# Performance work log

Measured on AMD Instinct MI355X. Metric: run time of the kernel, lower is better.

## Reference

```python
import jax, jax.numpy as jnp
import numpy as np

# SamplesLoss(loss='sinkhorn', p=1, blur=0.05): entropic regularization eps = blur**p = 0.05,
# debiased Sinkhorn divergence S(a,b) = OT(a,b) - 0.5*OT(a,a) - 0.5*OT(b,b).
EPS = 0.05
N_ITER = 50
N_POINTS = 32


def _cost(X, Y):
    # p=1 cost: Euclidean distance. X:[B,N,D] Y:[B,M,D] -> [B,N,M]
    d2 = jnp.sum((X[:, :, None, :] - Y[:, None, :, :]) ** 2, axis=-1)
    return jnp.sqrt(d2 + 1e-12)


def _ot(X, Y):
    # log-domain Sinkhorn with uniform weights; returns dual cost <mu,f>+<nu,g> per batch.
    B, N, _ = X.shape
    M = Y.shape[1]
    C = _cost(X, Y)  # [B,N,M]
    log_mu = jnp.full((B, N), -np.log(N), C.dtype)
    log_nu = jnp.full((B, M), -np.log(M), C.dtype)

    def body(carry, _):
        f, g = carry
        f = -EPS * jax.nn.logsumexp((g[:, None, :] - C) / EPS + log_nu[:, None, :], axis=2)
        g = -EPS * jax.nn.logsumexp((f[:, :, None] - C) / EPS + log_mu[:, :, None], axis=1)
        return (f, g), None

    init = (jnp.zeros((B, N), C.dtype), jnp.zeros((B, M), C.dtype))
    (f, g), _ = jax.lax.scan(body, init, None, length=N_ITER)
    return jnp.mean(f, axis=-1) + jnp.mean(g, axis=-1)  # uniform weights => mean


def _sinkhorn_div(X, Y):
    return _ot(X, Y) - 0.5 * _ot(X, X) - 0.5 * _ot(Y, Y)


def _encode(x, W, edge_index):
    # simple 1-layer GCN-style encoder: linear + mean neighbor aggregation + self, ReLU
    h = x @ W  # [n_nodes, emb_dim]
    src, dst = edge_index[0], edge_index[1]
    n = x.shape[0]
    agg = jax.ops.segment_sum(h[src], dst, num_segments=n)
    deg = jax.ops.segment_sum(jnp.ones(src.shape, h.dtype), dst, num_segments=n)
    return jax.nn.relu(h + agg / jnp.maximum(deg, 1.0)[:, None])


def setup_inputs() -> dict:
    key = jax.random.key(0)
    k1, k2, k3, k4, k5 = jax.random.split(key, 5)
    n_nodes, d_feat, emb_dim = 50000, 128, 256
    n_edges, n_pairs = 800000, 8192
    x = jax.random.normal(k1, (n_nodes, d_feat), jnp.float32)
    W = jax.random.normal(k2, (d_feat, emb_dim), jnp.float32) / np.sqrt(d_feat)
    edge_index = jax.random.randint(k3, (2, n_edges), 0, n_nodes, jnp.int64)
    pairs = jax.random.randint(k4, (2, n_pairs), 0, n_nodes, jnp.int64)
    graph_dist = jax.random.uniform(k5, (n_pairs,), jnp.float32, 1.0, 5.0)
    return {"x": x, "W": W, "edge_index": edge_index, "pairs": pairs,
            "graph_dist": graph_dist}


def reference(x, W, edge_index, pairs, graph_dist):
    z = _encode(x, W, edge_index)                       # [n_nodes, emb_dim]
    B = pairs.shape[1]
    Xa = z[pairs[0]].reshape(B, N_POINTS, -1)           # [B, n_points, space_dim]
    Xb = z[pairs[1]].reshape(B, N_POINTS, -1)
    distance = _sinkhorn_div(Xa, Xb)                    # = -score_pairs
    distortion = jnp.abs(distance - graph_dist) / graph_dist
    return jnp.mean(distortion)
```

## Files before the change

### kernel.cpp

```cpp
#include <hip/hip_runtime.h>

#define N_NODES 50000
#define N_EDGES 800000
#define N_PAIRS 8192
#define N_SLOTS (2 * N_PAIRS)
#define CAP     64

#define INV_EPS   20.0f
#define LOG2E_F   1.4426950408889634f
#define LN2_F     0.6931471805599453f
#define LN32_F    3.4657359027997265f
#define EPS_F     0.05f

typedef float f2 __attribute__((ext_vector_type(2)));

__global__ void k_mark(const int* __restrict__ pairs, int* __restrict__ flags) {
    int t = blockIdx.x * 256 + threadIdx.x;
    if (t < N_SLOTS) flags[pairs[t]] = 1;
}

__global__ __launch_bounds__(256) void k_scatter(
        const int* __restrict__ eidx, const int* __restrict__ flags,
        int* __restrict__ cnt, int* __restrict__ bucket) {
    int t = blockIdx.x * 256 + threadIdx.x;
    int dst = eidx[N_EDGES + t];
    if (!flags[dst]) return;
    int pos = atomicAdd(&cnt[dst], 1);
    if (pos < CAP) bucket[dst * CAP + pos] = eidx[t];
}

__global__ __launch_bounds__(256) void k_gemm(
        const int* __restrict__ pairs, const float* __restrict__ x,
        const int* __restrict__ cnt, const int* __restrict__ bucket,
        const float* __restrict__ W, float* __restrict__ Z) {
    __shared__ __align__(16) float Us[16 * 128];
    int sbase = blockIdx.x * 16;
    int t = threadIdx.x;
    int wave = t >> 6, lane = t & 63;

    #pragma unroll
    for (int rr = 0; rr < 4; ++rr) {
        int r = wave * 4 + rr;
        int node = pairs[sbase + r];
        int n = cnt[node];
        int m = (n < CAP) ? n : CAP;
        const int* bk = bucket + node * CAP;
        float ax = 0.0f, ay = 0.0f;
        int k = 0;
        for (; k + 4 <= m; k += 4) {
            int s0 = bk[k], s1 = bk[k + 1], s2 = bk[k + 2], s3 = bk[k + 3];
            float2 v0 = *(const float2*)(x + (size_t)s0 * 128 + lane * 2);
            float2 v1 = *(const float2*)(x + (size_t)s1 * 128 + lane * 2);
            float2 v2 = *(const float2*)(x + (size_t)s2 * 128 + lane * 2);
            float2 v3 = *(const float2*)(x + (size_t)s3 * 128 + lane * 2);
            ax += (v0.x + v1.x) + (v2.x + v3.x);
            ay += (v0.y + v1.y) + (v2.y + v3.y);
        }
        for (; k < m; ++k) {
            int s0 = bk[k];
            float2 v0 = *(const float2*)(x + (size_t)s0 * 128 + lane * 2);
            ax += v0.x;
            ay += v0.y;
        }
        float rdeg = 1.0f / fmaxf((float)n, 1.0f);
        float2 xv = *(const float2*)(x + (size_t)node * 128 + lane * 2);
        float2 o;
        o.x = fmaf(ax, rdeg, xv.x);
        o.y = fmaf(ay, rdeg, xv.y);
        *(float2*)(Us + r * 128 + lane * 2) = o;
    }
    __syncthreads();

    int jq = t & 63;
    int rq = t >> 6;
    float acc[4][4] = {};
    const float4* Wv = (const float4*)W;

    for (int k4 = 0; k4 < 32; ++k4) {
        float4 wv[4];
        #pragma unroll
        for (int i = 0; i < 4; ++i) wv[i] = Wv[(size_t)(k4 * 4 + i) * 64 + jq];
        #pragma unroll
        for (int r = 0; r < 4; ++r) {
            float4 uv = *(const float4*)(Us + (rq * 4 + r) * 128 + k4 * 4);
            float uk0 = uv.x, uk1 = uv.y, uk2 = uv.z, uk3 = uv.w;
            acc[r][0] = fmaf(uk0, wv[0].x, acc[r][0]);
            acc[r][1] = fmaf(uk0, wv[0].y, acc[r][1]);
            acc[r][2] = fmaf(uk0, wv[0].z, acc[r][2]);
            acc[r][3] = fmaf(uk0, wv[0].w, acc[r][3]);
            acc[r][0] = fmaf(uk1, wv[1].x, acc[r][0]);
            acc[r][1] = fmaf(uk1, wv[1].y, acc[r][1]);
            acc[r][2] = fmaf(uk1, wv[1].z, acc[r][2]);
            acc[r][3] = fmaf(uk1, wv[1].w, acc[r][3]);
            acc[r][0] = fmaf(uk2, wv[2].x, acc[r][0]);
            acc[r][1] = fmaf(uk2, wv[2].y, acc[r][1]);
            acc[r][2] = fmaf(uk2, wv[2].z, acc[r][2]);
            acc[r][3] = fmaf(uk2, wv[2].w, acc[r][3]);
            acc[r][0] = fmaf(uk3, wv[3].x, acc[r][0]);
            acc[r][1] = fmaf(uk3, wv[3].y, acc[r][1]);
            acc[r][2] = fmaf(uk3, wv[3].z, acc[r][2]);
            acc[r][3] = fmaf(uk3, wv[3].w, acc[r][3]);
        }
    }

    #pragma unroll
    for (int r = 0; r < 4; ++r) {
        float4 o;
        o.x = fmaxf(acc[r][0], 0.0f);
        o.y = fmaxf(acc[r][1], 0.0f);
        o.z = fmaxf(acc[r][2], 0.0f);
        o.w = fmaxf(acc[r][3], 0.0f);
        *(float4*)(Z + (size_t)(sbase + rq * 4 + r) * 256 + jq * 4) = o;
    }
}

__global__ __launch_bounds__(256) void k_sinkhorn(
        const float* __restrict__ Z, float* __restrict__ dist) {
    __shared__ __align__(16) float smem[4][640];

    int w = threadIdx.x >> 6;
    int lane = threadIdx.x & 63;
    const float CSCALE = -INV_EPS * LOG2E_F;
    const float CBIAS  = -LN32_F * LOG2E_F;

    if (blockIdx.x < 2048) {
        float* sX = &smem[w][0];
        float* sY = &smem[w][256];
        float* sf = &smem[w][512];
        float* sg = &smem[w][544];
        float* su = &smem[w][576];
        float* sv = &smem[w][608];

        int b = blockIdx.x * 4 + w;
        int sx = b, sy = N_PAIRS + b;

        *(float4*)(&sX[lane * 4]) = ((const float4*)(Z + (size_t)sx * 256))[lane];
        *(float4*)(&sY[lane * 4]) = ((const float4*)(Z + (size_t)sy * 256))[lane];
        sg[lane & 31] = 0.0f;

        int i_r = lane & 31, jh = lane >> 5;
        int j_c = lane & 31, ih = lane >> 5;

        f2 CrowV[8], CcolV[8];
        {
            const f2* xp = (const f2*)(&sX[i_r * 8]);
            f2 x0 = xp[0], x1 = xp[1], x2 = xp[2], x3 = xp[3];
            #pragma unroll
            for (int t = 0; t < 16; ++t) {
                int j = jh * 16 + t;
                const f2* yp = (const f2*)(&sY[j * 8]);
                f2 d, s2;
                d = x0 - yp[0]; s2 = d * d;
                d = x1 - yp[1]; s2 = __builtin_elementwise_fma(d, d, s2);
                d = x2 - yp[2]; s2 = __builtin_elementwise_fma(d, d, s2);
                d = x3 - yp[3]; s2 = __builtin_elementwise_fma(d, d, s2);
                float d2 = s2.x + s2.y + 1e-12f;
                CrowV[t >> 1][t & 1] = fmaf(__builtin_amdgcn_sqrtf(d2), CSCALE, CBIAS);
            }
            const f2* yp = (const f2*)(&sY[j_c * 8]);
            f2 y0 = yp[0], y1 = yp[1], y2 = yp[2], y3 = yp[3];
            #pragma unroll
            for (int t = 0; t < 16; ++t) {
                int i = ih * 16 + t;
                const f2* qp = (const f2*)(&sX[i * 8]);
                f2 d, s2;
                d = qp[0] - y0; s2 = d * d;
                d = qp[1] - y1; s2 = __builtin_elementwise_fma(d, d, s2);
                d = qp[2] - y2; s2 = __builtin_elementwise_fma(d, d, s2);
                d = qp[3] - y3; s2 = __builtin_elementwise_fma(d, d, s2);
                float d2 = s2.x + s2.y + 1e-12f;
                CcolV[t >> 1][t & 1] = fmaf(__builtin_amdgcn_sqrtf(d2), CSCALE, CBIAS);
            }
        }

        float ft = 0.0f, gt = 0.0f;

        #pragma unroll 1
        for (int it = 0; it < 2; ++it) {
            {
                const float4* gp = (const float4*)(&sg[jh * 16]);
                float4 G0 = gp[0], G1 = gp[1], G2 = gp[2], G3 = gp[3];
                f2 gv[8] = {f2{G0.x, G0.y}, f2{G0.z, G0.w}, f2{G1.x, G1.y}, f2{G1.z, G1.w},
                            f2{G2.x, G2.y}, f2{G2.z, G2.w}, f2{G3.x, G3.y}, f2{G3.z, G3.w}};
                f2 val[8], m2 = f2{-1e30f, -1e30f};
                #pragma unroll
                for (int t2 = 0; t2 < 8; ++t2) {
                    val[t2] = gv[t2] + CrowV[t2];
                    m2 = __builtin_elementwise_max(m2, val[t2]);
                }
                float m = fmaxf(m2.x, m2.y);
                m = fmaxf(m, __shfl_xor(m, 32));
                f2 mm = f2{m, m};
                float s0 = 0.0f, s1 = 0.0f;
                #pragma unroll
                for (int t2 = 0; t2 < 8; ++t2) {
                    f2 e = val[t2] - mm;
                    s0 += __builtin_amdgcn_exp2f(e.x);
                    s1 += __builtin_amdgcn_exp2f(e.y);
                }
                float s = s0 + s1;
                s += __shfl_xor(s, 32);
                ft = -(m + __builtin_amdgcn_logf(s));
            }
            sf[lane & 31] = ft;
            {
                const float4* fp = (const float4*)(&sf[ih * 16]);
                float4 F0 = fp[0], F1 = fp[1], F2 = fp[2], F3 = fp[3];
                f2 fv[8] = {f2{F0.x, F0.y}, f2{F0.z, F0.w}, f2{F1.x, F1.y}, f2{F1.z, F1.w},
                            f2{F2.x, F2.y}, f2{F2.z, F2.w}, f2{F3.x, F3.y}, f2{F3.z, F3.w}};
                f2 val[8], m2 = f2{-1e30f, -1e30f};
                #pragma unroll
                for (int t2 = 0; t2 < 8; ++t2) {
                    val[t2] = fv[t2] + CcolV[t2];
                    m2 = __builtin_elementwise_max(m2, val[t2]);
                }
                float m = fmaxf(m2.x, m2.y);
                m = fmaxf(m, __shfl_xor(m, 32));
                f2 mm = f2{m, m};
                float s0 = 0.0f, s1 = 0.0f;
                #pragma unroll
                for (int t2 = 0; t2 < 8; ++t2) {
                    f2 e = val[t2] - mm;
                    s0 += __builtin_amdgcn_exp2f(e.x);
                    s1 += __builtin_amdgcn_exp2f(e.y);
                }
                float s = s0 + s1;
                s += __shfl_xor(s, 32);
                gt = -(m + __builtin_amdgcn_logf(s));
            }
            sg[lane & 31] = gt;
        }

        f2 KR2[8], KC2[8];
        float ureg = 1.0f, vreg = 1.0f;

        auto absorb = [&]() {
            const float4* gp = (const float4*)(&sg[jh * 16]);
            float4 G0 = gp[0], G1 = gp[1], G2 = gp[2], G3 = gp[3];
            f2 gv[8] = {f2{G0.x, G0.y}, f2{G0.z, G0.w}, f2{G1.x, G1.y}, f2{G1.z, G1.w},
                        f2{G2.x, G2.y}, f2{G2.z, G2.w}, f2{G3.x, G3.y}, f2{G3.z, G3.w}};
            f2 ftv = f2{ft, ft};
            #pragma unroll
            for (int t2 = 0; t2 < 8; ++t2) {
                f2 a = (gv[t2] + CrowV[t2]) + ftv;
                KR2[t2].x = __builtin_amdgcn_exp2f(a.x);
                KR2[t2].y = __builtin_amdgcn_exp2f(a.y);
            }
            const float4* fp = (const float4*)(&sf[ih * 16]);
            float4 F0 = fp[0], F1 = fp[1], F2 = fp[2], F3 = fp[3];
            f2 fv[8] = {f2{F0.x, F0.y}, f2{F0.z, F0.w}, f2{F1.x, F1.y}, f2{F1.z, F1.w},
                        f2{F2.x, F2.y}, f2{F2.z, F2.w}, f2{F3.x, F3.y}, f2{F3.z, F3.w}};
            f2 gtv = f2{gt, gt};
            #pragma unroll
            for (int t2 = 0; t2 < 8; ++t2) {
                f2 a = (fv[t2] + CcolV[t2]) + gtv;
                KC2[t2].x = __builtin_amdgcn_exp2f(a.x);
                KC2[t2].y = __builtin_amdgcn_exp2f(a.y);
            }
            sv[lane & 31] = 1.0f;
            ureg = 1.0f;
            vreg = 1.0f;
        };

        const int blens[5] = {6, 6, 12, 12, 12};
        absorb();
        #pragma unroll 1
        for (int blk = 0; blk < 5; ++blk) {
            int L = blens[blk];
            #pragma unroll 2
            for (int s6 = 0; s6 < L; ++s6) {
                {
                    const float4* vp = (const float4*)(&sv[jh * 16]);
                    float4 A0 = vp[0], A1 = vp[1], A2 = vp[2], A3 = vp[3];
                    f2 acc0 = KR2[0] * f2{A0.x, A0.y};
                    f2 acc1 = KR2[1] * f2{A0.z, A0.w};
                    acc0 = __builtin_elementwise_fma(KR2[2], f2{A1.x, A1.y}, acc0);
                    acc1 = __builtin_elementwise_fma(KR2[3], f2{A1.z, A1.w}, acc1);
                    acc0 = __builtin_elementwise_fma(KR2[4], f2{A2.x, A2.y}, acc0);
                    acc1 = __builtin_elementwise_fma(KR2[5], f2{A2.z, A2.w}, acc1);
                    acc0 = __builtin_elementwise_fma(KR2[6], f2{A3.x, A3.y}, acc0);
                    acc1 = __builtin_elementwise_fma(KR2[7], f2{A3.z, A3.w}, acc1);
                    f2 a = acc0 + acc1;
                    float S = a.x + a.y;
                    S += __shfl_xor(S, 32);
                    ureg = __builtin_amdgcn_rcpf(S);
                }
                su[lane & 31] = ureg;
                {
                    const float4* up = (const float4*)(&su[ih * 16]);
                    float4 A0 = up[0], A1 = up[1], A2 = up[2], A3 = up[3];
                    f2 acc0 = KC2[0] * f2{A0.x, A0.y};
                    f2 acc1 = KC2[1] * f2{A0.z, A0.w};
                    acc0 = __builtin_elementwise_fma(KC2[2], f2{A1.x, A1.y}, acc0);
                    acc1 = __builtin_elementwise_fma(KC2[3], f2{A1.z, A1.w}, acc1);
                    acc0 = __builtin_elementwise_fma(KC2[4], f2{A2.x, A2.y}, acc0);
                    acc1 = __builtin_elementwise_fma(KC2[5], f2{A2.z, A2.w}, acc1);
                    acc0 = __builtin_elementwise_fma(KC2[6], f2{A3.x, A3.y}, acc0);
                    acc1 = __builtin_elementwise_fma(KC2[7], f2{A3.z, A3.w}, acc1);
                    f2 a = acc0 + acc1;
                    float T = a.x + a.y;
                    T += __shfl_xor(T, 32);
                    vreg = __builtin_amdgcn_rcpf(T);
                }
                sv[lane & 31] = vreg;
            }
            if (blk < 4) {
                ft += __builtin_amdgcn_logf(ureg);
                gt += __builtin_amdgcn_logf(vreg);
                sf[lane & 31] = ft;
                sg[lane & 31] = gt;
                absorb();
            }
        }
        ft += __builtin_amdgcn_logf(ureg);
        gt += __builtin_amdgcn_logf(vreg);

        float v = ft + gt;
        #pragma unroll
        for (int off = 32; off > 0; off >>= 1) v += __shfl_xor(v, off);
        if (lane == 0) {
            float cost = v * (EPS_F * LN2_F / 64.0f);
            unsafeAtomicAdd(&dist[b], cost);
        }
    } else {
        int h = lane >> 5, i = lane & 31;
        int P = (blockIdx.x - 2048) * 4 + w;
        int src = h ? (N_PAIRS + P) : P;

        float* sP  = &smem[w][h * 256];
        float* swv = &smem[w][512];
        float* spv = &smem[w][576];

        {
            const float4* zp = (const float4*)(Z + (size_t)src * 256);
            *(float4*)(&sP[i * 8])     = zp[i * 2];
            *(float4*)(&sP[i * 8 + 4]) = zp[i * 2 + 1];
        }

        f2 CV[16];
        {
            const f2* xp = (const f2*)(&sP[i * 8]);
            f2 x0 = xp[0], x1 = xp[1], x2 = xp[2], x3 = xp[3];
            #pragma unroll
            for (int j = 0; j < 32; ++j) {
                const f2* yp = (const f2*)(&sP[j * 8]);
                f2 d, s2;
                d = x0 - yp[0]; s2 = d * d;
                d = x1 - yp[1]; s2 = __builtin_elementwise_fma(d, d, s2);
                d = x2 - yp[2]; s2 = __builtin_elementwise_fma(d, d, s2);
                d = x3 - yp[3]; s2 = __builtin_elementwise_fma(d, d, s2);
                float d2 = s2.x + s2.y + 1e-12f;
                CV[j >> 1][j & 1] = fmaf(__builtin_amdgcn_sqrtf(d2), CSCALE, CBIAS);
            }
        }

        float pp = 0.0f, E = 1.0f, wcur = 1.0f, wprev = 1.0f;
        f2 KV[16];
        #pragma unroll
        for (int t = 0; t < 16; ++t) {
            KV[t].x = __builtin_amdgcn_exp2f(CV[t].x);
            KV[t].y = __builtin_amdgcn_exp2f(CV[t].y);
        }
        swv[lane] = 1.0f;

        const int blens[9] = {4, 12, 12, 12, 12, 12, 12, 12, 12};
        #pragma unroll 1
        for (int blk = 0; blk < 9; ++blk) {
            int L = blens[blk];
            #pragma unroll 2
            for (int s = 0; s < L; ++s) {
                const float4* wp = (const float4*)(&swv[h * 32]);
                float4 A0 = wp[0], A1 = wp[1], A2 = wp[2], A3 = wp[3];
                float4 A4 = wp[4], A5 = wp[5], A6 = wp[6], A7 = wp[7];
                f2 acc0 = KV[0] * f2{A0.x, A0.y};
                f2 acc1 = KV[1] * f2{A0.z, A0.w};
                acc0 = __builtin_elementwise_fma(KV[2],  f2{A1.x, A1.y}, acc0);
                acc1 = __builtin_elementwise_fma(KV[3],  f2{A1.z, A1.w}, acc1);
                acc0 = __builtin_elementwise_fma(KV[4],  f2{A2.x, A2.y}, acc0);
                acc1 = __builtin_elementwise_fma(KV[5],  f2{A2.z, A2.w}, acc1);
                acc0 = __builtin_elementwise_fma(KV[6],  f2{A3.x, A3.y}, acc0);
                acc1 = __builtin_elementwise_fma(KV[7],  f2{A3.z, A3.w}, acc1);
                acc0 = __builtin_elementwise_fma(KV[8],  f2{A4.x, A4.y}, acc0);
                acc1 = __builtin_elementwise_fma(KV[9],  f2{A4.z, A4.w}, acc1);
                acc0 = __builtin_elementwise_fma(KV[10], f2{A5.x, A5.y}, acc0);
                acc1 = __builtin_elementwise_fma(KV[11], f2{A5.z, A5.w}, acc1);
                acc0 = __builtin_elementwise_fma(KV[12], f2{A6.x, A6.y}, acc0);
                acc1 = __builtin_elementwise_fma(KV[13], f2{A6.z, A6.w}, acc1);
                acc0 = __builtin_elementwise_fma(KV[14], f2{A7.x, A7.y}, acc0);
                acc1 = __builtin_elementwise_fma(KV[15], f2{A7.z, A7.w}, acc1);
                f2 a = acc0 + acc1;
                float S = a.x + a.y;
                wprev = wcur;
                wcur = __builtin_amdgcn_rcpf(S) * E;
                swv[h * 32 + i] = wcur;
            }
            if (blk < 8) {
                pp += __builtin_amdgcn_logf(wcur);
                spv[lane] = pp;
                const float4* pv = (const float4*)(&spv[h * 32]);
                float4 P0 = pv[0], P1 = pv[1], P2 = pv[2], P3 = pv[3];
                float4 P4 = pv[4], P5 = pv[5], P6 = pv[6], P7 = pv[7];
                f2 pj[16] = {f2{P0.x,P0.y}, f2{P0.z,P0.w}, f2{P1.x,P1.y}, f2{P1.z,P1.w},
                             f2{P2.x,P2.y}, f2{P2.z,P2.w}, f2{P3.x,P3.y}, f2{P3.z,P3.w},
                             f2{P4.x,P4.y}, f2{P4.z,P4.w}, f2{P5.x,P5.y}, f2{P5.z,P5.w},
                             f2{P6.x,P6.y}, f2{P6.z,P6.w}, f2{P7.x,P7.y}, f2{P7.z,P7.w}};
                #pragma unroll
                for (int t = 0; t < 16; ++t) {
                    f2 a = pj[t] + CV[t];
                    KV[t].x = __builtin_amdgcn_exp2f(a.x);
                    KV[t].y = __builtin_amdgcn_exp2f(a.y);
                }
                E = __builtin_amdgcn_exp2f(-pp);
                wcur = 1.0f;
                swv[lane] = 1.0f;
            }
        }

        float zsum = 2.0f * pp + __builtin_amdgcn_logf(wprev)
                   + __builtin_amdgcn_logf(wcur);
        #pragma unroll
        for (int off = 16; off > 0; off >>= 1) zsum += __shfl_xor(zsum, off);
        if (i == 0) {
            float cost = zsum * (EPS_F * LN2_F / 32.0f);
            unsafeAtomicAdd(&dist[P], -0.5f * cost);
        }
    }
}

__global__ void k_finalize(const float* __restrict__ dist,
                           const float* __restrict__ gd, float* __restrict__ out) {
    __shared__ float red[256];
    float s = 0.0f;
    for (int i = threadIdx.x; i < N_PAIRS; i += 256) {
        float g = gd[i];
        s += fabsf(dist[i] - g) / g;
    }
    red[threadIdx.x] = s;
    __syncthreads();
    for (int o = 128; o > 0; o >>= 1) {
        if (threadIdx.x < o) red[threadIdx.x] += red[threadIdx.x + o];
        __syncthreads();
    }
    if (threadIdx.x == 0) out[0] = red[0] * (1.0f / N_PAIRS);
}

extern "C" void kernel_launch(void* const* d_in, const int* in_sizes, int n_in,
                              void* d_out, int out_size, void* d_ws, size_t ws_size,
                              hipStream_t stream) {
    const float* x    = (const float*)d_in[0];
    const float* W    = (const float*)d_in[1];
    const int*   eidx = (const int*)d_in[2];
    const int*   pair = (const int*)d_in[3];
    const float* gd   = (const float*)d_in[4];

    char* ws = (char*)d_ws;
    size_t off = 0;
    int*   cnt    = (int*)  (ws + off); off += (size_t)N_NODES * 4;
    int*   flags  = (int*)  (ws + off); off += (size_t)N_NODES * 4;
    float* dist   = (float*)(ws + off); off += (size_t)N_PAIRS * 4;
    size_t zero_bytes = off;
    int*   bucket = (int*)  (ws + off); off += (size_t)N_NODES * CAP * 4;
    float* Z      = (float*)(ws + off); off += (size_t)N_SLOTS * 256 * 4;

    hipMemsetAsync(d_ws, 0, zero_bytes, stream);
    k_mark    <<<(N_SLOTS + 255) / 256, 256, 0, stream>>>(pair, flags);
    k_scatter <<<N_EDGES / 256, 256, 0, stream>>>(eidx, flags, cnt, bucket);
    k_gemm    <<<N_SLOTS / 16, 256, 0, stream>>>(pair, x, cnt, bucket, W, Z);
    k_sinkhorn<<<4096, 256, 0, stream>>>(Z, dist);
    k_finalize<<<1, 256, 0, stream>>>(dist, gd, (float*)d_out);
}
```

Before: 261.6 us.

## Interleave OT and self-OT blocks; split self-OT row sums across half-wave partners

Blocks now alternate between cross-OT and self-OT work by blockIdx parity instead of running all cross blocks first, which spreads the two workload types evenly across CUs. In the self-OT path, each lane computes cost entries for its own row and for partner row i^16 over only half the columns, then combines the partial sums with a shuffle. Each iteration therefore reads half as much weight data from LDS per lane, at the cost of one cross-lane shuffle per iteration and extra sqrt work in setup.

```diff
diff --git a/kernel.cpp b/kernel.cpp
--- a/kernel.cpp
+++ b/kernel.cpp
@@ -123,7 +123,7 @@
     const float CSCALE = -INV_EPS * LOG2E_F;
     const float CBIAS  = -LN32_F * LOG2E_F;
 
-    if (blockIdx.x < 2048) {
+    if ((blockIdx.x & 1) == 0) {
         float* sX = &smem[w][0];
         float* sY = &smem[w][256];
         float* sf = &smem[w][512];
@@ -131,7 +131,7 @@
         float* su = &smem[w][576];
         float* sv = &smem[w][608];
 
-        int b = blockIdx.x * 4 + w;
+        int b = (blockIdx.x >> 1) * 4 + w;
         int sx = b, sy = N_PAIRS + b;
 
         *(float4*)(&sX[lane * 4]) = ((const float4*)(Z + (size_t)sx * 256))[lane];
@@ -324,7 +324,9 @@
         }
     } else {
         int h = lane >> 5, i = lane & 31;
-        int P = (blockIdx.x - 2048) * 4 + w;
+        int q = (i >> 4) & 1;
+        int ip = i ^ 16;
+        int P = (blockIdx.x >> 1) * 4 + w;
         int src = h ? (N_PAIRS + P) : P;
 
         float* sP  = &smem[w][h * 256];
@@ -337,29 +339,41 @@
             *(float4*)(&sP[i * 8 + 4]) = zp[i * 2 + 1];
         }
 
-        f2 CV[16];
+        f2 CA[8], CB[8];
         {
             const f2* xp = (const f2*)(&sP[i * 8]);
             f2 x0 = xp[0], x1 = xp[1], x2 = xp[2], x3 = xp[3];
+            const f2* bp = (const f2*)(&sP[ip * 8]);
+            f2 b0 = bp[0], b1 = bp[1], b2 = bp[2], b3 = bp[3];
             #pragma unroll
-            for (int j = 0; j < 32; ++j) {
+            for (int t = 0; t < 16; ++t) {
+                int j = q * 16 + t;
                 const f2* yp = (const f2*)(&sP[j * 8]);
+                f2 y0 = yp[0], y1 = yp[1], y2 = yp[2], y3 = yp[3];
                 f2 d, s2;
-                d = x0 - yp[0]; s2 = d * d;
-                d = x1 - yp[1]; s2 = __builtin_elementwise_fma(d, d, s2);
-                d = x2 - yp[2]; s2 = __builtin_elementwise_fma(d, d, s2);
-                d = x3 - yp[3]; s2 = __builtin_elementwise_fma(d, d, s2);
+                d = x0 - y0; s2 = d * d;
+                d = x1 - y1; s2 = __builtin_elementwise_fma(d, d, s2);
+                d = x2 - y2; s2 = __builtin_elementwise_fma(d, d, s2);
+                d = x3 - y3; s2 = __builtin_elementwise_fma(d, d, s2);
                 float d2 = s2.x + s2.y + 1e-12f;
-                CV[j >> 1][j & 1] = fmaf(__builtin_amdgcn_sqrtf(d2), CSCALE, CBIAS);
+                CA[t >> 1][t & 1] = fmaf(__builtin_amdgcn_sqrtf(d2), CSCALE, CBIAS);
+                d = b0 - y0; s2 = d * d;
+                d = b1 - y1; s2 = __builtin_elementwise_fma(d, d, s2);
+                d = b2 - y2; s2 = __builtin_elementwise_fma(d, d, s2);
+                d = b3 - y3; s2 = __builtin_elementwise_fma(d, d, s2);
+                float e2 = s2.x + s2.y + 1e-12f;
+                CB[t >> 1][t & 1] = fmaf(__builtin_amdgcn_sqrtf(e2), CSCALE, CBIAS);
             }
         }
 
         float pp = 0.0f, E = 1.0f, wcur = 1.0f, wprev = 1.0f;
-        f2 KV[16];
+        f2 KA[8], KB[8];
         #pragma unroll
-        for (int t = 0; t < 16; ++t) {
-            KV[t].x = __builtin_amdgcn_exp2f(CV[t].x);
-            KV[t].y = __builtin_amdgcn_exp2f(CV[t].y);
+        for (int t = 0; t < 8; ++t) {
+            KA[t].x = __builtin_amdgcn_exp2f(CA[t].x);
+            KA[t].y = __builtin_amdgcn_exp2f(CA[t].y);
+            KB[t].x = __builtin_amdgcn_exp2f(CB[t].x);
+            KB[t].y = __builtin_amdgcn_exp2f(CB[t].y);
         }
         swv[lane] = 1.0f;
 
@@ -369,27 +383,30 @@
             int L = blens[blk];
             #pragma unroll 2
             for (int s = 0; s < L; ++s) {
-                const float4* wp = (const float4*)(&swv[h * 32]);
+                const float4* wp = (const float4*)(&swv[h * 32 + q * 16]);
                 float4 A0 = wp[0], A1 = wp[1], A2 = wp[2], A3 = wp[3];
-                float4 A4 = wp[4], A5 = wp[5], A6 = wp[6], A7 = wp[7];
-                f2 acc0 = KV[0] * f2{A0.x, A0.y};
-                f2 acc1 = KV[1] * f2{A0.z, A0.w};
-                acc0 = __builtin_elementwise_fma(KV[2],  f2{A1.x, A1.y}, acc0);
-                acc1 = __builtin_elementwise_fma(KV[3],  f2{A1.z, A1.w}, acc1);
-                acc0 = __builtin_elementwise_fma(KV[4],  f2{A2.x, A2.y}, acc0);
-                acc1 = __builtin_elementwise_fma(KV[5],  f2{A2.z, A2.w}, acc1);
-                acc0 = __builtin_elementwise_fma(KV[6],  f2{A3.x, A3.y}, acc0);
-                acc1 = __builtin_elementwise_fma(KV[7],  f2{A3.z, A3.w}, acc1);
-                acc0 = __builtin_elementwise_fma(KV[8],  f2{A4.x, A4.y}, acc0);
-                acc1 = __builtin_elementwise_fma(KV[9],  f2{A4.z, A4.w}, acc1);
-                acc0 = __builtin_elementwise_fma(KV[10], f2{A5.x, A5.y}, acc0);
-                acc1 = __builtin_elementwise_fma(KV[11], f2{A5.z, A5.w}, acc1);
-                acc0 = __builtin_elementwise_fma(KV[12], f2{A6.x, A6.y}, acc0);
-                acc1 = __builtin_elementwise_fma(KV[13], f2{A6.z, A6.w}, acc1);
-                acc0 = __builtin_elementwise_fma(KV[14], f2{A7.x, A7.y}, acc0);
-                acc1 = __builtin_elementwise_fma(KV[15], f2{A7.z, A7.w}, acc1);
-                f2 a = acc0 + acc1;
-                float S = a.x + a.y;
+                f2 aA0 = KA[0] * f2{A0.x, A0.y};
+                f2 aA1 = KA[1] * f2{A0.z, A0.w};
+                f2 aB0 = KB[0] * f2{A0.x, A0.y};
+                f2 aB1 = KB[1] * f2{A0.z, A0.w};
+                aA0 = __builtin_elementwise_fma(KA[2], f2{A1.x, A1.y}, aA0);
+                aA1 = __builtin_elementwise_fma(KA[3], f2{A1.z, A1.w}, aA1);
+                aB0 = __builtin_elementwise_fma(KB[2], f2{A1.x, A1.y}, aB0);
+                aB1 = __builtin_elementwise_fma(KB[3], f2{A1.z, A1.w}, aB1);
+                aA0 = __builtin_elementwise_fma(KA[4], f2{A2.x, A2.y}, aA0);
+                aA1 = __builtin_elementwise_fma(KA[5], f2{A2.z, A2.w}, aA1);
+                aB0 = __builtin_elementwise_fma(KB[4], f2{A2.x, A2.y}, aB0);
+                aB1 = __builtin_elementwise_fma(KB[5], f2{A2.z, A2.w}, aB1);
+                aA0 = __builtin_elementwise_fma(KA[6], f2{A3.x, A3.y}, aA0);
+                aA1 = __builtin_elementwise_fma(KA[7], f2{A3.z, A3.w}, aA1);
+                aB0 = __builtin_elementwise_fma(KB[6], f2{A3.x, A3.y}, aB0);
+                aB1 = __builtin_elementwise_fma(KB[7], f2{A3.z, A3.w}, aB1);
+                f2 aa = aA0 + aA1;
+                f2 bb = aB0 + aB1;
+                float pa = aa.x + aa.y;
+                float pb = bb.x + bb.y;
+                float other = __shfl_xor(pb, 16);
+                float S = pa + other;
                 wprev = wcur;
                 wcur = __builtin_amdgcn_rcpf(S) * E;
                 swv[h * 32 + i] = wcur;
@@ -397,18 +414,18 @@
             if (blk < 8) {
                 pp += __builtin_amdgcn_logf(wcur);
                 spv[lane] = pp;
-                const float4* pv = (const float4*)(&spv[h * 32]);
+                const float4* pv = (const float4*)(&spv[h * 32 + q * 16]);
                 float4 P0 = pv[0], P1 = pv[1], P2 = pv[2], P3 = pv[3];
-                float4 P4 = pv[4], P5 = pv[5], P6 = pv[6], P7 = pv[7];
-                f2 pj[16] = {f2{P0.x,P0.y}, f2{P0.z,P0.w}, f2{P1.x,P1.y}, f2{P1.z,P1.w},
-                             f2{P2.x,P2.y}, f2{P2.z,P2.w}, f2{P3.x,P3.y}, f2{P3.z,P3.w},
-                             f2{P4.x,P4.y}, f2{P4.z,P4.w}, f2{P5.x,P5.y}, f2{P5.z,P5.w},
-                             f2{P6.x,P6.y}, f2{P6.z,P6.w}, f2{P7.x,P7.y}, f2{P7.z,P7.w}};
+                f2 pj[8] = {f2{P0.x,P0.y}, f2{P0.z,P0.w}, f2{P1.x,P1.y}, f2{P1.z,P1.w},
+                            f2{P2.x,P2.y}, f2{P2.z,P2.w}, f2{P3.x,P3.y}, f2{P3.z,P3.w}};
                 #pragma unroll
-                for (int t = 0; t < 16; ++t) {
-                    f2 a = pj[t] + CV[t];
-                    KV[t].x = __builtin_amdgcn_exp2f(a.x);
-                    KV[t].y = __builtin_amdgcn_exp2f(a.y);
+                for (int t = 0; t < 8; ++t) {
+                    f2 a = pj[t] + CA[t];
+                    KA[t].x = __builtin_amdgcn_exp2f(a.x);
+                    KA[t].y = __builtin_amdgcn_exp2f(a.y);
+                    f2 c = pj[t] + CB[t];
+                    KB[t].x = __builtin_amdgcn_exp2f(c.x);
+                    KB[t].y = __builtin_amdgcn_exp2f(c.y);
                 }
                 E = __builtin_amdgcn_exp2f(-pp);
                 wcur = 1.0f;
```

New measurement: 259.9 us. No clear change (-0.7%).
